# Kernel optimization log

Measured on AMD Instinct MI355X. Metric: run time of the kernel, lower is better.

The kernel has to match this reference:

```python
import jax, jax.numpy as jnp
import numpy as np

V, E, H, C_TAGS, B, T = 32000, 256, 200, 20, 64, 512
LN_EPS = 1e-5


def setup_inputs() -> dict:
    key = jax.random.key(0)
    ks = jax.random.split(key, 12)
    s = 0.05
    return {
        "words": jax.random.randint(ks[0], (B, T), 0, V),
        "seq_len": jax.random.randint(ks[1], (B,), T // 2, T + 1),
        "target": jax.random.randint(ks[2], (B, T), 0, C_TAGS),
        "embed_table": jax.random.normal(ks[3], (V, E)) * s,
        "ln_gamma": jnp.ones((E,)),
        "ln_beta": jnp.zeros((E,)),
        "w_ih_f": jax.random.normal(ks[4], (4 * H, E)) * s,
        "w_hh_f": jax.random.normal(ks[5], (4 * H, H)) * s,
        "b_f": jnp.zeros((4 * H,)),  # b_ih + b_hh folded together
        "w_ih_b": jax.random.normal(ks[6], (4 * H, E)) * s,
        "w_hh_b": jax.random.normal(ks[7], (4 * H, H)) * s,
        "b_b": jnp.zeros((4 * H,)),
        "fc_w": jax.random.normal(ks[8], (C_TAGS, 2 * H)) * s,
        "fc_b": jnp.zeros((C_TAGS,)),
        "trans": jax.random.normal(ks[9], (C_TAGS, C_TAGS)) * s,
        "start_scores": jax.random.normal(ks[10], (C_TAGS,)) * s,
        "end_scores": jax.random.normal(ks[11], (C_TAGS,)) * s,
    }


def _lstm_dir(x, m, w_ih, w_hh, b, reverse):
    """x: [T,B,E] time-major, m: [T,B] float mask. Packed-sequence semantics:
    carry only updates on valid steps (matters for the reverse direction)."""
    Hn = w_hh.shape[1]
    gates_x = jnp.einsum('tbe,ge->tbg', x, w_ih) + b  # [T,B,4H], batched GEMM

    def step(carry, xs):
        h, c = carry
        gx, mt = xs
        g = gx + h @ w_hh.T
        i, f, gg, o = jnp.split(g, 4, axis=-1)  # torch gate order i,f,g,o
        c_new = jax.nn.sigmoid(f) * c + jax.nn.sigmoid(i) * jnp.tanh(gg)
        h_new = jax.nn.sigmoid(o) * jnp.tanh(c_new)
        mt = mt[:, None]
        h = mt * h_new + (1.0 - mt) * h
        c = mt * c_new + (1.0 - mt) * c
        return (h, c), h

    init = (jnp.zeros((x.shape[1], Hn), x.dtype), jnp.zeros((x.shape[1], Hn), x.dtype))
    _, hs = jax.lax.scan(step, init, (gates_x, m), reverse=reverse)
    return hs  # [T,B,H]


def _crf_nll(logits, mask, target, trans, start, end):
    """Linear-chain CRF NLL with start/end transitions. logits [B,T,C] (emissions),
    mask [B,T] float, target [B,T] int. Returns per-sample loss [B]."""
    # --- log partition via forward algorithm (scan over time) ---
    alpha0 = start[None, :] + logits[:, 0]  # [B,C]
    emits = jnp.swapaxes(logits, 0, 1)[1:]  # [T-1,B,C]
    ms = jnp.swapaxes(mask, 0, 1)[1:]       # [T-1,B]

    def step(alpha, xs):
        emit, mt = xs
        scores = alpha[:, :, None] + trans[None, :, :] + emit[:, None, :]  # [B,C,C]
        new = jax.nn.logsumexp(scores, axis=1)
        alpha = jnp.where(mt[:, None] > 0, new, alpha)
        return alpha, None

    alpha, _ = jax.lax.scan(step, alpha0, (emits, ms))
    logZ = jax.nn.logsumexp(alpha + end[None, :], axis=1)  # [B]

    # --- gold path score ---
    emit_gold = jnp.take_along_axis(logits, target[..., None], axis=2)[..., 0]  # [B,T]
    emit_score = jnp.sum(emit_gold * mask, axis=1)
    trans_gold = trans[target[:, :-1], target[:, 1:]]  # [B,T-1]
    trans_score = jnp.sum(trans_gold * mask[:, 1:], axis=1)
    last_idx = jnp.sum(mask, axis=1).astype(jnp.int32) - 1
    last_tag = jnp.take_along_axis(target, last_idx[:, None], axis=1)[:, 0]
    gold = emit_score + trans_score + start[target[:, 0]] + end[last_tag]
    return logZ - gold


def reference(words, seq_len, target, embed_table, ln_gamma, ln_beta,
              w_ih_f, w_hh_f, b_f, w_ih_b, w_hh_b, b_b,
              fc_w, fc_b, trans, start_scores, end_scores):
    # Embedding + LayerNorm
    x = embed_table[words]  # [B,T,E]
    mu = x.mean(-1, keepdims=True)
    var = ((x - mu) ** 2).mean(-1, keepdims=True)
    x = (x - mu) * jax.lax.rsqrt(var + LN_EPS) * ln_gamma + ln_beta

    mask = (jnp.arange(x.shape[1])[None, :] < seq_len[:, None]).astype(x.dtype)  # [B,T]
    xt = jnp.swapaxes(x, 0, 1)       # [T,B,E]
    mt = jnp.swapaxes(mask, 0, 1)    # [T,B]

    # BiLSTM (num_layers=1)
    hf = _lstm_dir(xt, mt, w_ih_f, w_hh_f, b_f, reverse=False)
    hb = _lstm_dir(xt, mt, w_ih_b, w_hh_b, b_b, reverse=True)
    feats = jnp.swapaxes(jnp.concatenate([hf, hb], axis=-1), 0, 1)  # [B,T,2H]

    # fc + dropout (eval: identity) + log_softmax emissions
    feats = feats @ fc_w.T + fc_b
    logits = jax.nn.log_softmax(feats, axis=-1)

    loss = _crf_nll(logits, mask, target, trans, start_scores, end_scores)
    return loss.mean()
```

## Files before the change

### kernel.cpp

```cpp
#include <hip/hip_runtime.h>

#define TT 512
#define BB 64
#define EE 256
#define HH 200
#define GG 800
#define CC 20
#define MM (BB * TT)

typedef _Float16 f16x8 __attribute__((ext_vector_type(8)));
typedef float    f32x4 __attribute__((ext_vector_type(4)));
typedef _Float16 f16x2 __attribute__((ext_vector_type(2)));

#if __has_builtin(__builtin_amdgcn_mfma_f32_16x16x32_f16)
#define HAVE_MFMA_F16 1
#else
#define HAVE_MFMA_F16 0
#endif

__device__ __forceinline__ float bf2f(unsigned short u) {
  return __uint_as_float(((unsigned int)u) << 16);
}
__device__ __forceinline__ unsigned short f2bf(float f) {
  unsigned int u = __float_as_uint(f);
  return (unsigned short)((u + 0x7fffu + ((u >> 16) & 1u)) >> 16);
}
__device__ __forceinline__ float sigf(float x) { return 1.0f / (1.0f + __expf(-x)); }
__device__ __forceinline__ float tanhfast(float x) {
  return 1.0f - 2.0f / (__expf(2.0f * x) + 1.0f);
}
__device__ __forceinline__ f16x2 bfpair_to_h2(unsigned int p) {
  f16x2 r;
  r[0] = (_Float16)bf2f((unsigned short)(p & 0xffffu));
  r[1] = (_Float16)bf2f((unsigned short)(p >> 16));
  return r;
}
__device__ __forceinline__ float dot2acc(f16x2 a, f16x2 b, float c) {
#if __has_builtin(__builtin_amdgcn_fdot2)
  return __builtin_amdgcn_fdot2(a, b, c, false);
#else
  return c + (float)a[0] * (float)b[0] + (float)a[1] * (float)b[1];
#endif
}

#define NSEG 14
struct CvtArgs { const void* src[NSEG]; };
__constant__ const int cvt_cum[NSEG + 1] = {
    0, 8192000, 8192256, 8192512, 8397312, 8557312, 8558112,
    8762912, 8922912, 8923712, 8931712, 8931732, 8932132, 8932152, 8932172};

__global__ __launch_bounds__(256) void k_convert(CvtArgs a,
                                                 unsigned short* __restrict__ dst) {
  const bool f32mode = (((const unsigned int*)a.src[1])[0] == 0x3F800000u);
  int gi0 = (blockIdx.x * 256 + threadIdx.x) * 4;
#pragma unroll
  for (int r = 0; r < 4; ++r) {
    int gi = gi0 + r;
    if (gi >= cvt_cum[NSEG]) return;
    int seg = 0;
#pragma unroll
    for (int s = 1; s < NSEG; ++s) seg += (gi >= cvt_cum[s]) ? 1 : 0;
    int local = gi - cvt_cum[seg];
    unsigned short v;
    if (f32mode) v = f2bf(((const float*)a.src[seg])[local]);
    else         v = ((const unsigned short*)a.src[seg])[local];
    dst[gi] = v;
  }
}

__global__ __launch_bounds__(256) void k_embed_ln(
    const int* __restrict__ words, const unsigned short* __restrict__ etab,
    const unsigned short* __restrict__ gamma, const unsigned short* __restrict__ beta,
    unsigned short* __restrict__ x) {
  int m = blockIdx.x;
  int e = threadIdx.x;
  int w = words[m];
  float v = bf2f(etab[(size_t)w * EE + e]);
  float s = v, ss = v * v;
#pragma unroll
  for (int off = 32; off > 0; off >>= 1) {
    s += __shfl_xor(s, off, 64);
    ss += __shfl_xor(ss, off, 64);
  }
  __shared__ float red[2][4];
  int wv = e >> 6;
  if ((e & 63) == 0) { red[0][wv] = s; red[1][wv] = ss; }
  __syncthreads();
  float S = red[0][0] + red[0][1] + red[0][2] + red[0][3];
  float SS = red[1][0] + red[1][1] + red[1][2] + red[1][3];
  float mu = S * (1.0f / EE);
  float var = fmaxf(SS * (1.0f / EE) - mu * mu, 0.0f);
  float nrm = (v - mu) * rsqrtf(var + 1e-5f) * bf2f(gamma[e]) + bf2f(beta[e]);
  x[(size_t)m * EE + e] = f2bf(nrm);
}

#if HAVE_MFMA_F16
__global__ __launch_bounds__(256) void k_gates(
    const unsigned short* __restrict__ x,
    const unsigned short* __restrict__ wih_f, const unsigned short* __restrict__ wih_b,
    const unsigned short* __restrict__ bias_f, const unsigned short* __restrict__ bias_b,
    unsigned short* __restrict__ gates) {
  const int dir = blockIdx.z;
  const unsigned short* wih = dir ? wih_b : wih_f;
  const unsigned short* bias = dir ? bias_b : bias_f;
  const int m0 = blockIdx.x * 64;
  const int n0 = blockIdx.y * 64;
  __shared__ __align__(16) _Float16 As[64 * 32];
  __shared__ __align__(16) _Float16 Bs[64 * 32];
  const int tid = threadIdx.x;
  const int lane = tid & 63, wave = tid >> 6;
  const int wm = (wave >> 1) * 32, wn = (wave & 1) * 32;
  const int srow = tid >> 2, sq = tid & 3;
  const int mrow = lane & 15, q = lane >> 4;
  f32x4 acc[2][2] = {};
  for (int kk = 0; kk < EE; kk += 32) {
    union { int4 v; unsigned short u[8]; } ua, ub;
    ua.v = *(const int4*)(x + (size_t)(m0 + srow) * EE + kk + sq * 8);
    ub.v.x = 0; ub.v.y = 0; ub.v.z = 0; ub.v.w = 0;
    int n = n0 + srow;
    if (n < GG) ub.v = *(const int4*)(wih + (size_t)n * EE + kk + sq * 8);
    f16x8 af, bf;
#pragma unroll
    for (int r = 0; r < 8; ++r) {
      af[r] = (_Float16)bf2f(ua.u[r]);
      bf[r] = (_Float16)bf2f(ub.u[r]);
    }
    __syncthreads();
    *(f16x8*)(As + srow * 32 + sq * 8) = af;
    *(f16x8*)(Bs + srow * 32 + sq * 8) = bf;
    __syncthreads();
    f16x8 a0 = *(const f16x8*)(As + (wm + mrow) * 32 + q * 8);
    f16x8 a1 = *(const f16x8*)(As + (wm + 16 + mrow) * 32 + q * 8);
    f16x8 b0 = *(const f16x8*)(Bs + (wn + mrow) * 32 + q * 8);
    f16x8 b1 = *(const f16x8*)(Bs + (wn + 16 + mrow) * 32 + q * 8);
    acc[0][0] = __builtin_amdgcn_mfma_f32_16x16x32_f16(a0, b0, acc[0][0], 0, 0, 0);
    acc[0][1] = __builtin_amdgcn_mfma_f32_16x16x32_f16(a0, b1, acc[0][1], 0, 0, 0);
    acc[1][0] = __builtin_amdgcn_mfma_f32_16x16x32_f16(a1, b0, acc[1][0], 0, 0, 0);
    acc[1][1] = __builtin_amdgcn_mfma_f32_16x16x32_f16(a1, b1, acc[1][1], 0, 0, 0);
  }
#pragma unroll
  for (int im = 0; im < 2; ++im) {
#pragma unroll
    for (int in = 0; in < 2; ++in) {
      int n = n0 + wn + in * 16 + mrow;
      if (n < GG) {
        float bb = bf2f(bias[n]);
#pragma unroll
        for (int r = 0; r < 4; ++r) {
          int mg = m0 + wm + im * 16 + q * 4 + r;
          gates[((size_t)dir * MM + mg) * GG + n] = f2bf(acc[im][in][r] + bb);
        }
      }
    }
  }
}
#else
__global__ __launch_bounds__(256) void k_gates(
    const unsigned short* __restrict__ x,
    const unsigned short* __restrict__ wih_f, const unsigned short* __restrict__ wih_b,
    const unsigned short* __restrict__ bias_f, const unsigned short* __restrict__ bias_b,
    unsigned short* __restrict__ gates) {
  const int dir = blockIdx.z;
  const unsigned short* wih = dir ? wih_b : wih_f;
  const unsigned short* bias = dir ? bias_b : bias_f;
  const int m0 = blockIdx.x * 64;
  const int n0 = blockIdx.y * 64;
  for (int r = 0; r < 16; ++r) {
    int idx = threadIdx.x + 256 * r;
    int m = m0 + (idx >> 6), n = n0 + (idx & 63);
    if (n >= GG) continue;
    float acc = bf2f(bias[n]);
    const unsigned short* xr = x + (size_t)m * EE;
    const unsigned short* wr = wih + (size_t)n * EE;
    for (int k = 0; k < EE; ++k) acc += bf2f(xr[k]) * bf2f(wr[k]);
    gates[((size_t)dir * MM + m) * GG + n] = f2bf(acc);
  }
}
#endif

__global__ __launch_bounds__(832) void k_lstm(
    const unsigned short* __restrict__ gates,
    const unsigned short* __restrict__ whh_f, const unsigned short* __restrict__ whh_b,
    const int* __restrict__ seq_len,
    unsigned short* __restrict__ h_out) {
  const int b = blockIdx.x & (BB - 1);
  const int dir = blockIdx.x >> 6;
  const unsigned short* whh = dir ? whh_b : whh_f;
  const int tid = threadIdx.x;
  const int L = seq_len[b];
  __shared__ __align__(16) _Float16 hsh[HH];
  __shared__ float gbuf[GG];
  f16x2 w2[100];
  if (tid < GG) {
    const unsigned short* wr = whh + (size_t)tid * HH;
#pragma unroll
    for (int i = 0; i < 25; ++i) {
      int4 wvv = *(const int4*)(wr + i * 8);
      w2[4 * i + 0] = bfpair_to_h2((unsigned int)wvv.x);
      w2[4 * i + 1] = bfpair_to_h2((unsigned int)wvv.y);
      w2[4 * i + 2] = bfpair_to_h2((unsigned int)wvv.z);
      w2[4 * i + 3] = bfpair_to_h2((unsigned int)wvv.w);
    }
  }
  if (tid < HH) hsh[tid] = (_Float16)0.0f;
  float c_st = 0.0f, h_st = 0.0f;
  const unsigned short* gbase = gates + ((size_t)dir * MM + (size_t)b * TT) * GG + tid;
  unsigned short* hobase = h_out + (size_t)(dir * BB + b) * TT * HH;
  float gx_cur = 0.0f;
  if (tid < GG) {
    int t0 = dir ? (TT - 1) : 0;
    gx_cur = bf2f(gbase[(size_t)t0 * GG]);
  }
  __syncthreads();
  for (int s = 0; s < TT; ++s) {
    const int t = dir ? (TT - 1 - s) : s;
    if (tid < GG) {
      int sn = (s + 1 < TT) ? (s + 1) : s;
      int tn = dir ? (TT - 1 - sn) : sn;
      float gx_next = bf2f(gbase[(size_t)tn * GG]);
      float acc0 = gx_cur, acc1 = 0.0f;
#pragma unroll
      for (int i = 0; i < 25; ++i) {
        union { int4 v; f16x2 h[4]; } u;
        u.v = *(const int4*)(hsh + i * 8);
        acc0 = dot2acc(w2[4 * i + 0], u.h[0], acc0);
        acc1 = dot2acc(w2[4 * i + 1], u.h[1], acc1);
        acc0 = dot2acc(w2[4 * i + 2], u.h[2], acc0);
        acc1 = dot2acc(w2[4 * i + 3], u.h[3], acc1);
      }
      gbuf[tid] = acc0 + acc1;
      gx_cur = gx_next;
    }
    __syncthreads();
    if (tid < HH) {
      float gi = gbuf[tid], gf = gbuf[HH + tid];
      float gg = gbuf[2 * HH + tid], go = gbuf[3 * HH + tid];
      float cn = sigf(gf) * c_st + sigf(gi) * tanhfast(gg);
      float hn = sigf(go) * tanhfast(cn);
      if (t < L) { c_st = cn; h_st = hn; }
      hsh[tid] = (_Float16)h_st;
      hobase[(size_t)t * HH + tid] = f2bf(h_st);
    }
    __syncthreads();
  }
}

__global__ __launch_bounds__(256) void k_fc(
    const unsigned short* __restrict__ h_out,
    const unsigned short* __restrict__ fc_w, const unsigned short* __restrict__ fc_b,
    float* __restrict__ logits) {
  __shared__ __align__(16) unsigned short hsh[4][2 * HH];
  const int wv = threadIdx.x >> 6, lane = threadIdx.x & 63;
  const int m = blockIdx.x * 4 + wv;
  if (lane < 25) {
    *(int4*)&hsh[wv][lane * 8] = *(const int4*)(h_out + (size_t)m * HH + lane * 8);
  } else if (lane < 50) {
    *(int4*)&hsh[wv][HH + (lane - 25) * 8] =
        *(const int4*)(h_out + (size_t)MM * HH + (size_t)m * HH + (lane - 25) * 8);
  }
  __syncthreads();
  float s = -3.0e38f;
  if (lane < CC) {
    s = bf2f(fc_b[lane]);
    const unsigned short* wrow = fc_w + lane * 2 * HH;
    for (int jj = 0; jj < 50; ++jj) {
      union { int4 v; unsigned short u[8]; } hw, ww;
      hw.v = *(const int4*)&hsh[wv][jj * 8];
      ww.v = *(const int4*)(wrow + jj * 8);
#pragma unroll
      for (int r = 0; r < 8; ++r) s += bf2f(hw.u[r]) * bf2f(ww.u[r]);
    }
  }
  float mx = s;
#pragma unroll
  for (int off = 32; off > 0; off >>= 1) mx = fmaxf(mx, __shfl_xor(mx, off, 64));
  float ex = (lane < CC) ? __expf(s - mx) : 0.0f;
  float sm = ex;
#pragma unroll
  for (int off = 32; off > 0; off >>= 1) sm += __shfl_xor(sm, off, 64);
  if (lane < CC) logits[(size_t)m * CC + lane] = s - mx - __logf(sm);
}

__global__ __launch_bounds__(64) void k_crf(
    const float* __restrict__ logits, const int* __restrict__ target,
    const int* __restrict__ seq_len, const unsigned short* __restrict__ trans,
    const unsigned short* __restrict__ startv, const unsigned short* __restrict__ endv,
    float* __restrict__ loss_b) {
  const int b = blockIdx.x, lane = threadIdx.x;
  const int L = seq_len[b];
  const int* tg = target + b * TT;
  const float* lg = logits + (size_t)b * TT * CC;
  float tcol[CC];
#pragma unroll
  for (int i = 0; i < CC; ++i) tcol[i] = (lane < CC) ? bf2f(trans[i * CC + lane]) : 0.0f;
  float g = 0.0f;
  for (int t = lane; t < TT; t += 64) {
    if (t < L) {
      g += lg[t * CC + tg[t]];
      if (t >= 1) g += bf2f(trans[tg[t - 1] * CC + tg[t]]);
    }
  }
#pragma unroll
  for (int off = 32; off > 0; off >>= 1) g += __shfl_xor(g, off, 64);
  float alpha = (lane < CC) ? (bf2f(startv[lane]) + lg[lane]) : -3.0e38f;
  for (int t = 1; t < L; ++t) {
    float e = (lane < CC) ? lg[t * CC + lane] : 0.0f;
    float sc[CC];
#pragma unroll
    for (int i = 0; i < CC; ++i) sc[i] = __shfl(alpha, i, 64) + tcol[i];
    float mx = sc[0];
#pragma unroll
    for (int i = 1; i < CC; ++i) mx = fmaxf(mx, sc[i]);
    float sm = 0.0f;
#pragma unroll
    for (int i = 0; i < CC; ++i) sm += __expf(sc[i] - mx);
    float na = mx + __logf(sm) + e;
    if (lane < CC) alpha = na;
  }
  float v = (lane < CC) ? (alpha + bf2f(endv[lane])) : -3.0e38f;
  float mx = v;
#pragma unroll
  for (int off = 32; off > 0; off >>= 1) mx = fmaxf(mx, __shfl_xor(mx, off, 64));
  float ex = (lane < CC) ? __expf(v - mx) : 0.0f;
#pragma unroll
  for (int off = 32; off > 0; off >>= 1) ex += __shfl_xor(ex, off, 64);
  if (lane == 0) {
    float logZ = mx + __logf(ex);
    float gold = g + bf2f(startv[tg[0]]) + bf2f(endv[tg[L - 1]]);
    loss_b[b] = logZ - gold;
  }
}

__global__ __launch_bounds__(64) void k_mean(const float* __restrict__ loss_b,
                                             unsigned int* __restrict__ out) {
  float v = loss_b[threadIdx.x];
#pragma unroll
  for (int off = 32; off > 0; off >>= 1) v += __shfl_xor(v, off, 64);
  if (threadIdx.x == 0) {
    float mean = v * (1.0f / BB);
    unsigned int lo = (unsigned int)f2bf(mean);
    unsigned int hi = __float_as_uint(mean) >> 16;
    out[0] = (hi << 16) | lo;
  }
}

extern "C" void kernel_launch(void* const* d_in, const int* in_sizes, int n_in,
                              void* d_out, int out_size, void* d_ws, size_t ws_size,
                              hipStream_t stream) {
  const int* words   = (const int*)d_in[0];
  const int* seq_len = (const int*)d_in[1];
  const int* target  = (const int*)d_in[2];

  char* ws = (char*)d_ws;
  const size_t x_off      = 0;
  const size_t gates_off  = x_off + 16777216;
  const size_t h_off      = gates_off + 104857600;
  const size_t logits_off = h_off + 26214400;
  const size_t loss_off   = logits_off + 2621440;
  const size_t cvt_off    = loss_off + 256;
  unsigned short* x      = (unsigned short*)(ws + x_off);
  unsigned short* gatesb = (unsigned short*)(ws + gates_off);
  unsigned short* h_out  = (unsigned short*)(ws + h_off);
  float* logits          = (float*)(ws + logits_off);
  float* loss_b          = (float*)(ws + loss_off);
  unsigned short* wcvt   = (unsigned short*)(ws + cvt_off);

  unsigned short* etab_c  = wcvt + 0;
  unsigned short* gamma_c = wcvt + 8192000;
  unsigned short* beta_c  = wcvt + 8192256;
  unsigned short* wih_f_c = wcvt + 8192512;
  unsigned short* whh_f_c = wcvt + 8397312;
  unsigned short* b_f_c   = wcvt + 8557312;
  unsigned short* wih_b_c = wcvt + 8558112;
  unsigned short* whh_b_c = wcvt + 8762912;
  unsigned short* b_b_c   = wcvt + 8922912;
  unsigned short* fc_w_c  = wcvt + 8923712;
  unsigned short* fc_b_c  = wcvt + 8931712;
  unsigned short* trans_c = wcvt + 8931732;
  unsigned short* start_c = wcvt + 8932132;
  unsigned short* end_c   = wcvt + 8932152;

  CvtArgs ca;
  for (int i = 0; i < NSEG; ++i) ca.src[i] = d_in[3 + i];
  const int total_cvt = 8932172;
  k_convert<<<(total_cvt + 1023) / 1024, 256, 0, stream>>>(ca, wcvt);

  k_embed_ln<<<MM, 256, 0, stream>>>(words, etab_c, gamma_c, beta_c, x);
  k_gates<<<dim3(MM / 64, 13, 2), 256, 0, stream>>>(x, wih_f_c, wih_b_c, b_f_c, b_b_c, gatesb);
  k_lstm<<<128, 832, 0, stream>>>(gatesb, whh_f_c, whh_b_c, seq_len, h_out);
  k_fc<<<MM / 4, 256, 0, stream>>>(h_out, fc_w_c, fc_b_c, logits);
  k_crf<<<BB, 64, 0, stream>>>(logits, target, seq_len, trans_c, start_c, end_c, loss_b);
  k_mean<<<1, 64, 0, stream>>>(loss_b, (unsigned int*)d_out);
}
```

Before: 1.140 ms.

## Batch LSTM recurrence over 16 sequences per block with MFMA and padded weights

The recurrent step now runs as an MFMA matmul. Each of 8 blocks handles 16 batch elements in one direction, in place of one block per sequence doing scalar fdot2 products. The gate GEMM output is re-laid out time-major with batch innermost and gate rows padded to 208 per gate, so each step reads contiguous gate slices. A prep kernel pre-converts and pads W_ih/W_hh to fp16, and the embedding table is read directly instead of being converted to bf16 every call. The risk is that only 8 blocks run the serial recurrence, which leaves most CUs idle, and that W_hh is re-read from global/L2 every step.

```diff
diff --git a/kernel.cpp b/kernel.cpp
--- a/kernel.cpp
+++ b/kernel.cpp
@@ -7,16 +7,11 @@
 #define GG 800
 #define CC 20
 #define MM (BB * TT)
+#define NP 832
+#define KP 224
 
 typedef _Float16 f16x8 __attribute__((ext_vector_type(8)));
 typedef float    f32x4 __attribute__((ext_vector_type(4)));
-typedef _Float16 f16x2 __attribute__((ext_vector_type(2)));
-
-#if __has_builtin(__builtin_amdgcn_mfma_f32_16x16x32_f16)
-#define HAVE_MFMA_F16 1
-#else
-#define HAVE_MFMA_F16 0
-#endif
 
 __device__ __forceinline__ float bf2f(unsigned short u) {
   return __uint_as_float(((unsigned int)u) << 16);
@@ -29,29 +24,16 @@
 __device__ __forceinline__ float tanhfast(float x) {
   return 1.0f - 2.0f / (__expf(2.0f * x) + 1.0f);
 }
-__device__ __forceinline__ f16x2 bfpair_to_h2(unsigned int p) {
-  f16x2 r;
-  r[0] = (_Float16)bf2f((unsigned short)(p & 0xffffu));
-  r[1] = (_Float16)bf2f((unsigned short)(p >> 16));
-  return r;
-}
-__device__ __forceinline__ float dot2acc(f16x2 a, f16x2 b, float c) {
-#if __has_builtin(__builtin_amdgcn_fdot2)
-  return __builtin_amdgcn_fdot2(a, b, c, false);
-#else
-  return c + (float)a[0] * (float)b[0] + (float)a[1] * (float)b[1];
-#endif
-}
-
-#define NSEG 14
+
+#define NSEG 13
 struct CvtArgs { const void* src[NSEG]; };
 __constant__ const int cvt_cum[NSEG + 1] = {
-    0, 8192000, 8192256, 8192512, 8397312, 8557312, 8558112,
-    8762912, 8922912, 8923712, 8931712, 8931732, 8932132, 8932152, 8932172};
+    0, 256, 512, 205312, 365312, 366112, 570912, 730912,
+    731712, 739712, 739732, 740132, 740152, 740172};
 
 __global__ __launch_bounds__(256) void k_convert(CvtArgs a,
                                                  unsigned short* __restrict__ dst) {
-  const bool f32mode = (((const unsigned int*)a.src[1])[0] == 0x3F800000u);
+  const bool f32mode = (((const unsigned int*)a.src[0])[0] == 0x3F800000u);
   int gi0 = (blockIdx.x * 256 + threadIdx.x) * 4;
 #pragma unroll
   for (int r = 0; r < 4; ++r) {
@@ -68,14 +50,39 @@
   }
 }
 
+__global__ __launch_bounds__(256) void k_prep(
+    const unsigned short* __restrict__ wih_f, const unsigned short* __restrict__ wih_b,
+    const unsigned short* __restrict__ whh_f, const unsigned short* __restrict__ whh_b,
+    _Float16* __restrict__ wihP, _Float16* __restrict__ whhP) {
+  const int dir = blockIdx.x / NP;
+  const int n = blockIdx.x % NP;
+  const int e = threadIdx.x;
+  const int g = n / 208, j = n % 208;
+  const bool rowok = (j < 200);
+  const unsigned short* wih = dir ? wih_b : wih_f;
+  const unsigned short* whh = dir ? whh_b : whh_f;
+  _Float16 vi = (_Float16)0.0f;
+  if (rowok) vi = (_Float16)bf2f(wih[(size_t)(g * 200 + j) * EE + e]);
+  wihP[((size_t)dir * NP + n) * EE + e] = vi;
+  if (e < KP) {
+    _Float16 vh = (_Float16)0.0f;
+    if (rowok && e < HH) vh = (_Float16)bf2f(whh[(size_t)(g * 200 + j) * HH + e]);
+    whhP[((size_t)dir * NP + n) * KP + e] = vh;
+  }
+}
+
 __global__ __launch_bounds__(256) void k_embed_ln(
-    const int* __restrict__ words, const unsigned short* __restrict__ etab,
+    const int* __restrict__ words, const void* __restrict__ etab_raw,
+    const unsigned int* __restrict__ probe,
     const unsigned short* __restrict__ gamma, const unsigned short* __restrict__ beta,
     unsigned short* __restrict__ x) {
+  const bool f32m = (probe[0] == 0x3F800000u);
   int m = blockIdx.x;
   int e = threadIdx.x;
   int w = words[m];
-  float v = bf2f(etab[(size_t)w * EE + e]);
+  size_t idx = (size_t)w * EE + e;
+  float v = f32m ? ((const float*)etab_raw)[idx]
+                 : bf2f(((const unsigned short*)etab_raw)[idx]);
   float s = v, ss = v * v;
 #pragma unroll
   for (int off = 32; off > 0; off >>= 1) {
@@ -91,19 +98,19 @@
   float mu = S * (1.0f / EE);
   float var = fmaxf(SS * (1.0f / EE) - mu * mu, 0.0f);
   float nrm = (v - mu) * rsqrtf(var + 1e-5f) * bf2f(gamma[e]) + bf2f(beta[e]);
-  x[(size_t)m * EE + e] = f2bf(nrm);
-}
-
-#if HAVE_MFMA_F16
+  int row = ((m & 511) << 6) | (m >> 9);
+  x[(size_t)row * EE + e] = f2bf(nrm);
+}
+
 __global__ __launch_bounds__(256) void k_gates(
     const unsigned short* __restrict__ x,
-    const unsigned short* __restrict__ wih_f, const unsigned short* __restrict__ wih_b,
+    const _Float16* __restrict__ wihP,
     const unsigned short* __restrict__ bias_f, const unsigned short* __restrict__ bias_b,
-    unsigned short* __restrict__ gates) {
+    unsigned short* __restrict__ G2) {
   const int dir = blockIdx.z;
-  const unsigned short* wih = dir ? wih_b : wih_f;
   const unsigned short* bias = dir ? bias_b : bias_f;
-  const int m0 = blockIdx.x * 64;
+  const int t = blockIdx.x;
+  const int m0 = t * 64;
   const int n0 = blockIdx.y * 64;
   __shared__ __align__(16) _Float16 As[64 * 32];
   __shared__ __align__(16) _Float16 Bs[64 * 32];
@@ -114,20 +121,15 @@
   const int mrow = lane & 15, q = lane >> 4;
   f32x4 acc[2][2] = {};
   for (int kk = 0; kk < EE; kk += 32) {
-    union { int4 v; unsigned short u[8]; } ua, ub;
+    union { int4 v; unsigned short u[8]; } ua;
     ua.v = *(const int4*)(x + (size_t)(m0 + srow) * EE + kk + sq * 8);
-    ub.v.x = 0; ub.v.y = 0; ub.v.z = 0; ub.v.w = 0;
-    int n = n0 + srow;
-    if (n < GG) ub.v = *(const int4*)(wih + (size_t)n * EE + kk + sq * 8);
-    f16x8 af, bf;
-#pragma unroll
-    for (int r = 0; r < 8; ++r) {
-      af[r] = (_Float16)bf2f(ua.u[r]);
-      bf[r] = (_Float16)bf2f(ub.u[r]);
-    }
+    int4 bv = *(const int4*)(wihP + ((size_t)dir * NP + n0 + srow) * EE + kk + sq * 8);
+    f16x8 af;
+#pragma unroll
+    for (int r = 0; r < 8; ++r) af[r] = (_Float16)bf2f(ua.u[r]);
     __syncthreads();
     *(f16x8*)(As + srow * 32 + sq * 8) = af;
-    *(f16x8*)(Bs + srow * 32 + sq * 8) = bf;
+    *(int4*)(Bs + srow * 32 + sq * 8) = bv;
     __syncthreads();
     f16x8 a0 = *(const f16x8*)(As + (wm + mrow) * 32 + q * 8);
     f16x8 a1 = *(const f16x8*)(As + (wm + 16 + mrow) * 32 + q * 8);
@@ -143,103 +145,85 @@
 #pragma unroll
     for (int in = 0; in < 2; ++in) {
       int n = n0 + wn + in * 16 + mrow;
-      if (n < GG) {
-        float bb = bf2f(bias[n]);
-#pragma unroll
-        for (int r = 0; r < 4; ++r) {
-          int mg = m0 + wm + im * 16 + q * 4 + r;
-          gates[((size_t)dir * MM + mg) * GG + n] = f2bf(acc[im][in][r] + bb);
-        }
-      }
+      int g = n / 208, j = n - g * 208;
+      float bb = (j < 200) ? bf2f(bias[g * 200 + j]) : 0.0f;
+      int b0v = wm + im * 16 + q * 4;
+      unsigned int lo = (unsigned int)f2bf(acc[im][in][0] + bb) |
+                        ((unsigned int)f2bf(acc[im][in][1] + bb) << 16);
+      unsigned int hi = (unsigned int)f2bf(acc[im][in][2] + bb) |
+                        ((unsigned int)f2bf(acc[im][in][3] + bb) << 16);
+      uint2 pk; pk.x = lo; pk.y = hi;
+      *(uint2*)(G2 + (((size_t)dir * TT + t) * NP + n) * 64 + b0v) = pk;
     }
   }
 }
-#else
-__global__ __launch_bounds__(256) void k_gates(
-    const unsigned short* __restrict__ x,
-    const unsigned short* __restrict__ wih_f, const unsigned short* __restrict__ wih_b,
-    const unsigned short* __restrict__ bias_f, const unsigned short* __restrict__ bias_b,
-    unsigned short* __restrict__ gates) {
-  const int dir = blockIdx.z;
-  const unsigned short* wih = dir ? wih_b : wih_f;
-  const unsigned short* bias = dir ? bias_b : bias_f;
-  const int m0 = blockIdx.x * 64;
-  const int n0 = blockIdx.y * 64;
-  for (int r = 0; r < 16; ++r) {
-    int idx = threadIdx.x + 256 * r;
-    int m = m0 + (idx >> 6), n = n0 + (idx & 63);
-    if (n >= GG) continue;
-    float acc = bf2f(bias[n]);
-    const unsigned short* xr = x + (size_t)m * EE;
-    const unsigned short* wr = wih + (size_t)n * EE;
-    for (int k = 0; k < EE; ++k) acc += bf2f(xr[k]) * bf2f(wr[k]);
-    gates[((size_t)dir * MM + m) * GG + n] = f2bf(acc);
-  }
-}
-#endif
-
-__global__ __launch_bounds__(832) void k_lstm(
-    const unsigned short* __restrict__ gates,
-    const unsigned short* __restrict__ whh_f, const unsigned short* __restrict__ whh_b,
+
+__global__ __launch_bounds__(512)
+__attribute__((amdgpu_waves_per_eu(2, 2)))
+void k_lstm(
+    const unsigned short* __restrict__ G2,
+    const _Float16* __restrict__ whhP,
     const int* __restrict__ seq_len,
     unsigned short* __restrict__ h_out) {
-  const int b = blockIdx.x & (BB - 1);
-  const int dir = blockIdx.x >> 6;
-  const unsigned short* whh = dir ? whh_b : whh_f;
+  const int dir = blockIdx.x >> 2;
+  const int bg = blockIdx.x & 3;
   const int tid = threadIdx.x;
-  const int L = seq_len[b];
-  __shared__ __align__(16) _Float16 hsh[HH];
-  __shared__ float gbuf[GG];
-  f16x2 w2[100];
-  if (tid < GG) {
-    const unsigned short* wr = whh + (size_t)tid * HH;
-#pragma unroll
-    for (int i = 0; i < 25; ++i) {
-      int4 wvv = *(const int4*)(wr + i * 8);
-      w2[4 * i + 0] = bfpair_to_h2((unsigned int)wvv.x);
-      w2[4 * i + 1] = bfpair_to_h2((unsigned int)wvv.y);
-      w2[4 * i + 2] = bfpair_to_h2((unsigned int)wvv.z);
-      w2[4 * i + 3] = bfpair_to_h2((unsigned int)wvv.w);
-    }
-  }
-  if (tid < HH) hsh[tid] = (_Float16)0.0f;
-  float c_st = 0.0f, h_st = 0.0f;
-  const unsigned short* gbase = gates + ((size_t)dir * MM + (size_t)b * TT) * GG + tid;
-  unsigned short* hobase = h_out + (size_t)(dir * BB + b) * TT * HH;
-  float gx_cur = 0.0f;
-  if (tid < GG) {
-    int t0 = dir ? (TT - 1) : 0;
-    gx_cur = bf2f(gbase[(size_t)t0 * GG]);
-  }
+  const int wv = tid >> 6;
+  const int lane = tid & 63;
+  const int nn = lane & 15;
+  const int q = lane >> 4;
+  const int ut0 = (wv < 5) ? 2 * wv : 10 + (wv - 5);
+  const int nut = (wv < 5) ? 2 : 1;
+  __shared__ __align__(16) _Float16 hbuf[2][16][232];
+  for (int i = tid; i < 2 * 16 * 232; i += 512) ((_Float16*)hbuf)[i] = (_Float16)0.0f;
+  const int mb = q * 4;
+  int Lb[4];
+#pragma unroll
+  for (int r = 0; r < 4; ++r) Lb[r] = seq_len[bg * 16 + mb + r];
+  float c_st[2][4] = {{0, 0, 0, 0}, {0, 0, 0, 0}};
+  float h_st[2][4] = {{0, 0, 0, 0}, {0, 0, 0, 0}};
+  const size_t g2dir = (size_t)dir * TT * NP * 64;
   __syncthreads();
   for (int s = 0; s < TT; ++s) {
     const int t = dir ? (TT - 1 - s) : s;
-    if (tid < GG) {
-      int sn = (s + 1 < TT) ? (s + 1) : s;
-      int tn = dir ? (TT - 1 - sn) : sn;
-      float gx_next = bf2f(gbase[(size_t)tn * GG]);
-      float acc0 = gx_cur, acc1 = 0.0f;
-#pragma unroll
-      for (int i = 0; i < 25; ++i) {
-        union { int4 v; f16x2 h[4]; } u;
-        u.v = *(const int4*)(hsh + i * 8);
-        acc0 = dot2acc(w2[4 * i + 0], u.h[0], acc0);
-        acc1 = dot2acc(w2[4 * i + 1], u.h[1], acc1);
-        acc0 = dot2acc(w2[4 * i + 2], u.h[2], acc0);
-        acc1 = dot2acc(w2[4 * i + 3], u.h[3], acc1);
+    const int p = s & 1;
+    f16x8 A[7];
+#pragma unroll
+    for (int k = 0; k < 7; ++k)
+      A[k] = *(const f16x8*)(&hbuf[p][nn][k * 32 + q * 8]);
+#pragma unroll
+    for (int u = 0; u < 2; ++u) {
+      if (u >= nut) break;
+      const int ut = ut0 + u;
+      const int unit = ut * 16 + nn;
+      f32x4 acc[4];
+      uint2 gx[4];
+#pragma unroll
+      for (int g = 0; g < 4; ++g) {
+        const int nrow = g * 208 + unit;
+        gx[g] = *(const uint2*)(G2 + g2dir + ((size_t)t * NP + nrow) * 64 + bg * 16 + mb);
+        acc[g][0] = 0.0f; acc[g][1] = 0.0f; acc[g][2] = 0.0f; acc[g][3] = 0.0f;
+        const _Float16* wr = whhP + ((size_t)dir * NP + nrow) * KP;
+#pragma unroll
+        for (int k = 0; k < 7; ++k) {
+          f16x8 Bf = *(const f16x8*)(wr + k * 32 + q * 8);
+          acc[g] = __builtin_amdgcn_mfma_f32_16x16x32_f16(A[k], Bf, acc[g], 0, 0, 0);
+        }
       }
-      gbuf[tid] = acc0 + acc1;
-      gx_cur = gx_next;
-    }
-    __syncthreads();
-    if (tid < HH) {
-      float gi = gbuf[tid], gf = gbuf[HH + tid];
-      float gg = gbuf[2 * HH + tid], go = gbuf[3 * HH + tid];
-      float cn = sigf(gf) * c_st + sigf(gi) * tanhfast(gg);
-      float hn = sigf(go) * tanhfast(cn);
-      if (t < L) { c_st = cn; h_st = hn; }
-      hsh[tid] = (_Float16)h_st;
-      hobase[(size_t)t * HH + tid] = f2bf(h_st);
+#pragma unroll
+      for (int r = 0; r < 4; ++r) {
+        float gi = acc[0][r] + bf2f(((const unsigned short*)&gx[0])[r]);
+        float gf = acc[1][r] + bf2f(((const unsigned short*)&gx[1])[r]);
+        float gg = acc[2][r] + bf2f(((const unsigned short*)&gx[2])[r]);
+        float go = acc[3][r] + bf2f(((const unsigned short*)&gx[3])[r]);
+        float cn = sigf(gf) * c_st[u][r] + sigf(gi) * tanhfast(gg);
+        float hn = sigf(go) * tanhfast(cn);
+        if (t < Lb[r]) { c_st[u][r] = cn; h_st[u][r] = hn; }
+        float hv = h_st[u][r];
+        hbuf[p ^ 1][mb + r][unit] = (_Float16)hv;
+        if (unit < HH)
+          h_out[((size_t)(dir * BB + bg * 16 + mb + r) * TT + t) * HH + unit] = f2bf(hv);
+      }
     }
     __syncthreads();
   }
@@ -353,41 +337,44 @@
 
   char* ws = (char*)d_ws;
   const size_t x_off      = 0;
-  const size_t gates_off  = x_off + 16777216;
-  const size_t h_off      = gates_off + 104857600;
-  const size_t logits_off = h_off + 26214400;
-  const size_t loss_off   = logits_off + 2621440;
-  const size_t cvt_off    = loss_off + 256;
+  const size_t g2_off     = 16777216;
+  const size_t h_off      = 125829120;
+  const size_t logits_off = 152043520;
+  const size_t loss_off   = 154664960;
+  const size_t cvt_off    = 154665216;
+  const size_t wihp_off   = 156145664;
+  const size_t whhp_off   = 156997632;
   unsigned short* x      = (unsigned short*)(ws + x_off);
-  unsigned short* gatesb = (unsigned short*)(ws + gates_off);
+  unsigned short* G2     = (unsigned short*)(ws + g2_off);
   unsigned short* h_out  = (unsigned short*)(ws + h_off);
   float* logits          = (float*)(ws + logits_off);
   float* loss_b          = (float*)(ws + loss_off);
   unsigned short* wcvt   = (unsigned short*)(ws + cvt_off);
-
-  unsigned short* etab_c  = wcvt + 0;
-  unsigned short* gamma_c = wcvt + 8192000;
-  unsigned short* beta_c  = wcvt + 8192256;
-  unsigned short* wih_f_c = wcvt + 8192512;
-  unsigned short* whh_f_c = wcvt + 8397312;
-  unsigned short* b_f_c   = wcvt + 8557312;
-  unsigned short* wih_b_c = wcvt + 8558112;
-  unsigned short* whh_b_c = wcvt + 8762912;
-  unsigned short* b_b_c   = wcvt + 8922912;
-  unsigned short* fc_w_c  = wcvt + 8923712;
-  unsigned short* fc_b_c  = wcvt + 8931712;
-  unsigned short* trans_c = wcvt + 8931732;
-  unsigned short* start_c = wcvt + 8932132;
-  unsigned short* end_c   = wcvt + 8932152;
+  _Float16* wihP         = (_Float16*)(ws + wihp_off);
+  _Float16* whhP         = (_Float16*)(ws + whhp_off);
+
+  unsigned short* gamma_c = wcvt + 0;
+  unsigned short* beta_c  = wcvt + 256;
+  unsigned short* wih_f_c = wcvt + 512;
+  unsigned short* whh_f_c = wcvt + 205312;
+  unsigned short* b_f_c   = wcvt + 365312;
+  unsigned short* wih_b_c = wcvt + 366112;
+  unsigned short* whh_b_c = wcvt + 570912;
+  unsigned short* b_b_c   = wcvt + 730912;
+  unsigned short* fc_w_c  = wcvt + 731712;
+  unsigned short* fc_b_c  = wcvt + 739712;
+  unsigned short* trans_c = wcvt + 739732;
+  unsigned short* start_c = wcvt + 740132;
+  unsigned short* end_c   = wcvt + 740152;
 
   CvtArgs ca;
-  for (int i = 0; i < NSEG; ++i) ca.src[i] = d_in[3 + i];
-  const int total_cvt = 8932172;
-  k_convert<<<(total_cvt + 1023) / 1024, 256, 0, stream>>>(ca, wcvt);
-
-  k_embed_ln<<<MM, 256, 0, stream>>>(words, etab_c, gamma_c, beta_c, x);
-  k_gates<<<dim3(MM / 64, 13, 2), 256, 0, stream>>>(x, wih_f_c, wih_b_c, b_f_c, b_b_c, gatesb);
-  k_lstm<<<128, 832, 0, stream>>>(gatesb, whh_f_c, whh_b_c, seq_len, h_out);
+  for (int i = 0; i < NSEG; ++i) ca.src[i] = d_in[4 + i];
+  k_convert<<<(740172 + 1023) / 1024, 256, 0, stream>>>(ca, wcvt);
+  k_prep<<<2 * NP, 256, 0, stream>>>(wih_f_c, wih_b_c, whh_f_c, whh_b_c, wihP, whhP);
+  k_embed_ln<<<MM, 256, 0, stream>>>(words, d_in[3], (const unsigned int*)d_in[4],
+                                     gamma_c, beta_c, x);
+  k_gates<<<dim3(TT, 13, 2), 256, 0, stream>>>(x, wihP, b_f_c, b_b_c, G2);
+  k_lstm<<<8, 512, 0, stream>>>(G2, whhP, seq_len, h_out);
   k_fc<<<MM / 4, 256, 0, stream>>>(h_out, fc_w_c, fc_b_c, logits);
   k_crf<<<BB, 64, 0, stream>>>(logits, target, seq_len, trans_c, start_c, end_c, loss_b);
   k_mean<<<1, 64, 0, stream>>>(loss_b, (unsigned int*)d_out);
```

Measured after the change: 4.032 ms. 3.54x slower.
